# Performance work log

Measured on AMD Instinct MI355X. Metric: run time of the kernel, lower is better.

Reference implementation:

```python
import jax, jax.numpy as jnp
import numpy as np

TEMPERATURE = 0.07
BALANCE = 1.0


def _l2norm(x, eps=1e-12):
    return x / jnp.maximum(jnp.linalg.norm(x, axis=1, keepdims=True), eps)


def setup_inputs() -> dict:
    key = jax.random.key(0)
    k1, k2 = jax.random.split(key)
    B, K, D = 32768, 8192, 384
    features = _l2norm(jax.random.normal(k1, (B, D), dtype=jnp.float32))
    centroids = jax.random.normal(k2, (K, D), dtype=jnp.float32)
    return {"features": features, "centroids": centroids}


def reference(features, centroids):
    # centroids: [K, D] learnable; features: [B, D] sampled batch (L2-normalized)
    c = _l2norm(centroids)
    # chunked matmul + exp + row-max in source == single fused GEMM+exp+max here
    prod_exp = jnp.exp(jnp.matmul(features, c.T) / TEMPERATURE)  # [B, K]
    pos_k = jnp.argmax(prod_exp, axis=1)                          # [B] int
    prod_exp_pos = jnp.max(prod_exp, axis=1)                      # [B]
    # centroid-centroid similarity; first operand is detached in source
    cent_exp = jnp.exp(jnp.matmul(jax.lax.stop_gradient(c), c.T) / TEMPERATURE)  # [K, K]
    cent_sum = jnp.sum(cent_exp, axis=0)                          # [K]
    J = jnp.log(prod_exp_pos) - jnp.log(prod_exp_pos + cent_sum[pos_k] * BALANCE)
    return -jnp.mean(J)
```

## Files before the change

### kernel.cpp

```cpp
#include <hip/hip_runtime.h>
#include <math.h>

constexpr int B = 32768;
constexpr int K = 8192;
constexpr int D = 384;
constexpr float INV_T = 1.0f / 0.07f;

constexpr int TILE_B = 24 * 64 * 16;

typedef int    int8v    __attribute__((ext_vector_type(8)));
typedef float  floatx16 __attribute__((ext_vector_type(16)));

__global__ __launch_bounds__(64) void normalize_k(const float* __restrict__ cent,
                                                  unsigned char* __restrict__ cbs) {
    const int row = blockIdx.x, lane = threadIdx.x;
    const float* src = cent + (size_t)row * D;
    float4 x = {0.f, 0.f, 0.f, 0.f}, y = {0.f, 0.f, 0.f, 0.f};
    if (lane < 48) {
        x = *(const float4*)(src + lane * 8);
        y = *(const float4*)(src + lane * 8 + 4);
    }
    float ss = x.x * x.x + x.y * x.y + x.z * x.z + x.w * x.w
             + y.x * y.x + y.y * y.y + y.z * y.z + y.w * y.w;
#pragma unroll
    for (int off = 32; off > 0; off >>= 1) ss += __shfl_down(ss, off, 64);
    ss = __shfl(ss, 0, 64);
    const float inv = 1.0f / fmaxf(sqrtf(ss), 1e-12f);
    if (lane < 48) {
        int w0 = __builtin_amdgcn_cvt_pk_fp8_f32(x.x * inv, x.y * inv, 0, false);
        w0 = __builtin_amdgcn_cvt_pk_fp8_f32(x.z * inv, x.w * inv, w0, true);
        int w1 = __builtin_amdgcn_cvt_pk_fp8_f32(y.x * inv, y.y * inv, 0, false);
        w1 = __builtin_amdgcn_cvt_pk_fp8_f32(y.z * inv, y.w * inv, w1, true);
        char* dst = (char*)cbs + (size_t)(row >> 6) * TILE_B
                  + ((size_t)(lane >> 1) * 64 + (row & 63)) * 16 + (lane & 1) * 8;
        *(int2*)dst = make_int2(w0, w1);
    }
}

__device__ __forceinline__ int8v read_frag(const char* base, int t, int half) {
    const uint4 b0 = *(const uint4*)(base + (4 * t + 2 * half) * 1024);
    const uint4 b1 = *(const uint4*)(base + (4 * t + 2 * half + 1) * 1024);
    int8v f;
    f[0] = b0.x; f[1] = b0.y; f[2] = b0.z; f[3] = b0.w;
    f[4] = b1.x; f[5] = b1.y; f[6] = b1.z; f[7] = b1.w;
    return f;
}

__global__ __launch_bounds__(256, 2) void centsum_k(const unsigned char* __restrict__ cbs,
                                                    float* __restrict__ cent_sum) {
    const int tid = threadIdx.x, lane = tid & 63, wave = tid >> 6;
    const int wm = wave >> 1, wn = wave & 1;
    const int l31 = lane & 31, half = lane >> 5;
    const int rb = blockIdx.x >> 3, ch = blockIdx.x & 7;
    const int stag = (rb & 3) * 4;

    int8v afr[2][6];
#pragma unroll
    for (int s = 0; s < 2; ++s) {
        const char* abase = (const char*)cbs + (size_t)(rb * 2 + wm) * TILE_B
                          + (s * 32 + l31) * 16;
#pragma unroll
        for (int t = 0; t < 6; ++t) afr[s][t] = read_frag(abase, t, half);
    }

    float rs[2][16];
#pragma unroll
    for (int s = 0; s < 2; ++s)
#pragma unroll
        for (int r = 0; r < 16; ++r) rs[s][r] = 0.f;

#pragma unroll 2
    for (int it = 0; it < 16; ++it) {
        const int tile = ch * 16 + ((stag + it) & 15);
        const char* gb = (const char*)cbs + (size_t)tile * TILE_B
                       + (wn * 32 + l31) * 16;
        int8v bfr[6];
#pragma unroll
        for (int t = 0; t < 6; ++t) bfr[t] = read_frag(gb, t, half);
        floatx16 acc0, acc1;
#pragma unroll
        for (int r = 0; r < 16; ++r) { acc0[r] = 0.f; acc1[r] = 0.f; }
#pragma unroll
        for (int t = 0; t < 6; ++t) {
            acc0 = __builtin_amdgcn_mfma_scale_f32_32x32x64_f8f6f4(
                       afr[0][t], bfr[t], acc0, 0, 0, 0, 127, 0, 127);
            acc1 = __builtin_amdgcn_mfma_scale_f32_32x32x64_f8f6f4(
                       afr[1][t], bfr[t], acc1, 0, 0, 0, 127, 0, 127);
        }
#pragma unroll
        for (int r = 0; r < 16; ++r) {
            rs[0][r] += __expf(acc0[r] * INV_T);
            rs[1][r] += __expf(acc1[r] * INV_T);
        }
    }

#pragma unroll
    for (int s = 0; s < 2; ++s)
#pragma unroll
        for (int r = 0; r < 16; ++r) {
            float v = rs[s][r];
#pragma unroll
            for (int off = 1; off < 32; off <<= 1) v += __shfl_xor(v, off, 64);
            if (l31 == 0) {
                const int rowl = (r & 3) + 8 * (r >> 2) + 4 * half;
                atomicAdd(&cent_sum[rb * 128 + wm * 64 + s * 32 + rowl], v);
            }
        }
}

__global__ __launch_bounds__(256, 2) void rowmax_k(const float* __restrict__ f,
                                                   const unsigned char* __restrict__ cbs,
                                                   float* __restrict__ row_max2,
                                                   int* __restrict__ row_arg2) {
    __shared__ float rv[128 * 2];
    __shared__ int   ri[128 * 2];
    const int tid = threadIdx.x, lane = tid & 63, wave = tid >> 6;
    const int wm = wave >> 1, wn = wave & 1;
    const int l31 = lane & 31, half = lane >> 5;
    const int rb = blockIdx.x >> 1, ch = blockIdx.x & 1;
    const int stag = (rb & 7) * 8;

    int8v afr[2][6];
    const int rowbase = rb * 128 + wm * 64;
#pragma unroll
    for (int s = 0; s < 2; ++s) {
        const float* arow = f + (size_t)(rowbase + s * 32 + l31) * D;
#pragma unroll
        for (int t = 0; t < 6; ++t) {
            const float* p = arow + t * 64 + half * 32;
            int8v a;
#pragma unroll
            for (int q = 0; q < 8; ++q) {
                const float4 v = *(const float4*)(p + q * 4);
                int w = __builtin_amdgcn_cvt_pk_fp8_f32(v.x, v.y, 0, false);
                w = __builtin_amdgcn_cvt_pk_fp8_f32(v.z, v.w, w, true);
                a[q] = w;
            }
            afr[s][t] = a;
        }
    }

    float bv[2][16];
    int   bi[2][16];
#pragma unroll
    for (int s = 0; s < 2; ++s)
#pragma unroll
        for (int r = 0; r < 16; ++r) { bv[s][r] = -INFINITY; bi[s][r] = 0; }

#pragma unroll 2
    for (int it = 0; it < 64; ++it) {
        const int tile = ch * 64 + ((stag + it) & 63);
        const char* gb = (const char*)cbs + (size_t)tile * TILE_B
                       + (wn * 32 + l31) * 16;
        int8v bfr[6];
#pragma unroll
        for (int t = 0; t < 6; ++t) bfr[t] = read_frag(gb, t, half);
        floatx16 acc0, acc1;
#pragma unroll
        for (int r = 0; r < 16; ++r) { acc0[r] = 0.f; acc1[r] = 0.f; }
#pragma unroll
        for (int t = 0; t < 6; ++t) {
            acc0 = __builtin_amdgcn_mfma_scale_f32_32x32x64_f8f6f4(
                       afr[0][t], bfr[t], acc0, 0, 0, 0, 127, 0, 127);
            acc1 = __builtin_amdgcn_mfma_scale_f32_32x32x64_f8f6f4(
                       afr[1][t], bfr[t], acc1, 0, 0, 0, 127, 0, 127);
        }
        const int curCol = tile * 64 + wn * 32 + l31;
#pragma unroll
        for (int r = 0; r < 16; ++r) {
            if (acc0[r] > bv[0][r]) { bv[0][r] = acc0[r]; bi[0][r] = curCol; }
            if (acc1[r] > bv[1][r]) { bv[1][r] = acc1[r]; bi[1][r] = curCol; }
        }
    }

#pragma unroll
    for (int s = 0; s < 2; ++s)
#pragma unroll
        for (int r = 0; r < 16; ++r) {
            float v = bv[s][r]; int ix = bi[s][r];
#pragma unroll
            for (int off = 1; off < 32; off <<= 1) {
                const float ov = __shfl_xor(v, off, 64);
                const int   oi = __shfl_xor(ix, off, 64);
                if (ov > v || (ov == v && oi < ix)) { v = ov; ix = oi; }
            }
            bv[s][r] = v; bi[s][r] = ix;
        }

    if (l31 == 0) {
#pragma unroll
        for (int s = 0; s < 2; ++s)
#pragma unroll
            for (int r = 0; r < 16; ++r) {
                const int row = wm * 64 + s * 32 + (r & 3) + 8 * (r >> 2) + 4 * half;
                rv[row * 2 + wn] = bv[s][r];
                ri[row * 2 + wn] = bi[s][r];
            }
    }
    __syncthreads();
    if (tid < 128) {
        const float v0 = rv[tid * 2], v1 = rv[tid * 2 + 1];
        const int   i0 = ri[tid * 2], i1 = ri[tid * 2 + 1];
        const bool take1 = (v1 > v0) || (v1 == v0 && i1 < i0);
        row_max2[(size_t)(rb * 128 + tid) * 2 + ch] = take1 ? v1 : v0;
        row_arg2[(size_t)(rb * 128 + tid) * 2 + ch] = take1 ? i1 : i0;
    }
}

__global__ __launch_bounds__(256) void loss_k(const float* __restrict__ row_max2,
                                              const int* __restrict__ row_arg2,
                                              const float* __restrict__ cent_sum,
                                              float* __restrict__ out) {
    __shared__ float red[256];
    const int tid = threadIdx.x;
    float s = 0.f;
    for (int b = blockIdx.x * 256 + tid; b < B; b += gridDim.x * 256) {
        const float m0 = row_max2[(size_t)b * 2], m1 = row_max2[(size_t)b * 2 + 1];
        const bool take1 = m1 > m0;
        const float m = take1 ? m1 : m0;
        const int ix = row_arg2[(size_t)b * 2 + (take1 ? 1 : 0)];
        s += log1pf(cent_sum[ix] * expf(-m * INV_T));
    }
    red[tid] = s;
    __syncthreads();
    for (int off = 128; off > 0; off >>= 1) {
        if (tid < off) red[tid] += red[tid + off];
        __syncthreads();
    }
    if (tid == 0) atomicAdd(out, red[0] / (float)B);
}

extern "C" void kernel_launch(void* const* d_in, const int* in_sizes, int n_in,
                              void* d_out, int out_size, void* d_ws, size_t ws_size,
                              hipStream_t stream) {
    const float* features  = (const float*)d_in[0];
    const float* centroids = (const float*)d_in[1];
    float* out = (float*)d_out;

    char* ws = (char*)d_ws;
    unsigned char* cbs = (unsigned char*)ws;
    float* cent_sum = (float*)(ws + (size_t)(K / 64) * TILE_B);
    float* row_max2 = cent_sum + K;
    int*   row_arg2 = (int*)(row_max2 + 2 * B);

    hipMemsetAsync(cent_sum, 0, K * sizeof(float), stream);
    hipMemsetAsync(out, 0, sizeof(float), stream);
    normalize_k<<<K, 64, 0, stream>>>(centroids, cbs);
    centsum_k<<<(K / 128) * 8, 256, 0, stream>>>(cbs, cent_sum);
    rowmax_k<<<(B / 128) * 2, 256, 0, stream>>>(features, cbs, row_max2, row_arg2);
    loss_k<<<64, 256, 0, stream>>>(row_max2, row_arg2, cent_sum, out);
}
```

Measured before the change: 240.5 us.

## Double per-block row tile to 256 so each B fragment feeds four MFMAs

```diff
diff --git a/kernel.cpp b/kernel.cpp
--- a/kernel.cpp
+++ b/kernel.cpp
@@ -46,7 +46,7 @@
     return f;
 }
 
-__global__ __launch_bounds__(256, 2) void centsum_k(const unsigned char* __restrict__ cbs,
+__global__ __launch_bounds__(256, 1) void centsum_k(const unsigned char* __restrict__ cbs,
                                                     float* __restrict__ cent_sum) {
     const int tid = threadIdx.x, lane = tid & 63, wave = tid >> 6;
     const int wm = wave >> 1, wn = wave & 1;
@@ -54,22 +54,22 @@
     const int rb = blockIdx.x >> 3, ch = blockIdx.x & 7;
     const int stag = (rb & 3) * 4;
 
-    int8v afr[2][6];
-#pragma unroll
-    for (int s = 0; s < 2; ++s) {
-        const char* abase = (const char*)cbs + (size_t)(rb * 2 + wm) * TILE_B
-                          + (s * 32 + l31) * 16;
+    int8v afr[4][6];
+#pragma unroll
+    for (int s = 0; s < 4; ++s) {
+        const char* abase = (const char*)cbs
+                          + (size_t)(rb * 4 + wm * 2 + (s >> 1)) * TILE_B
+                          + ((s & 1) * 32 + l31) * 16;
 #pragma unroll
         for (int t = 0; t < 6; ++t) afr[s][t] = read_frag(abase, t, half);
     }
 
-    float rs[2][16];
-#pragma unroll
-    for (int s = 0; s < 2; ++s)
+    float rs[4][16];
+#pragma unroll
+    for (int s = 0; s < 4; ++s)
 #pragma unroll
         for (int r = 0; r < 16; ++r) rs[s][r] = 0.f;
 
-#pragma unroll 2
     for (int it = 0; it < 16; ++it) {
         const int tile = ch * 16 + ((stag + it) & 15);
         const char* gb = (const char*)cbs + (size_t)tile * TILE_B
@@ -77,25 +77,26 @@
         int8v bfr[6];
 #pragma unroll
         for (int t = 0; t < 6; ++t) bfr[t] = read_frag(gb, t, half);
-        floatx16 acc0, acc1;
-#pragma unroll
-        for (int r = 0; r < 16; ++r) { acc0[r] = 0.f; acc1[r] = 0.f; }
+        floatx16 acc[4];
+#pragma unroll
+        for (int s = 0; s < 4; ++s)
+#pragma unroll
+            for (int r = 0; r < 16; ++r) acc[s][r] = 0.f;
 #pragma unroll
         for (int t = 0; t < 6; ++t) {
-            acc0 = __builtin_amdgcn_mfma_scale_f32_32x32x64_f8f6f4(
-                       afr[0][t], bfr[t], acc0, 0, 0, 0, 127, 0, 127);
-            acc1 = __builtin_amdgcn_mfma_scale_f32_32x32x64_f8f6f4(
-                       afr[1][t], bfr[t], acc1, 0, 0, 0, 127, 0, 127);
-        }
-#pragma unroll
-        for (int r = 0; r < 16; ++r) {
-            rs[0][r] += __expf(acc0[r] * INV_T);
-            rs[1][r] += __expf(acc1[r] * INV_T);
-        }
-    }
-
-#pragma unroll
-    for (int s = 0; s < 2; ++s)
+#pragma unroll
+            for (int s = 0; s < 4; ++s)
+                acc[s] = __builtin_amdgcn_mfma_scale_f32_32x32x64_f8f6f4(
+                             afr[s][t], bfr[t], acc[s], 0, 0, 0, 127, 0, 127);
+        }
+#pragma unroll
+        for (int s = 0; s < 4; ++s)
+#pragma unroll
+            for (int r = 0; r < 16; ++r) rs[s][r] += __expf(acc[s][r] * INV_T);
+    }
+
+#pragma unroll
+    for (int s = 0; s < 4; ++s)
 #pragma unroll
         for (int r = 0; r < 16; ++r) {
             float v = rs[s][r];
@@ -103,27 +104,27 @@
             for (int off = 1; off < 32; off <<= 1) v += __shfl_xor(v, off, 64);
             if (l31 == 0) {
                 const int rowl = (r & 3) + 8 * (r >> 2) + 4 * half;
-                atomicAdd(&cent_sum[rb * 128 + wm * 64 + s * 32 + rowl], v);
-            }
-        }
-}
-
-__global__ __launch_bounds__(256, 2) void rowmax_k(const float* __restrict__ f,
+                atomicAdd(&cent_sum[rb * 256 + wm * 128 + s * 32 + rowl], v);
+            }
+        }
+}
+
+__global__ __launch_bounds__(256, 1) void rowmax_k(const float* __restrict__ f,
                                                    const unsigned char* __restrict__ cbs,
                                                    float* __restrict__ row_max2,
                                                    int* __restrict__ row_arg2) {
-    __shared__ float rv[128 * 2];
-    __shared__ int   ri[128 * 2];
+    __shared__ float rv[256 * 2];
+    __shared__ int   ri[256 * 2];
     const int tid = threadIdx.x, lane = tid & 63, wave = tid >> 6;
     const int wm = wave >> 1, wn = wave & 1;
     const int l31 = lane & 31, half = lane >> 5;
     const int rb = blockIdx.x >> 1, ch = blockIdx.x & 1;
     const int stag = (rb & 7) * 8;
 
-    int8v afr[2][6];
-    const int rowbase = rb * 128 + wm * 64;
-#pragma unroll
-    for (int s = 0; s < 2; ++s) {
+    int8v afr[4][6];
+    const int rowbase = rb * 256 + wm * 128;
+#pragma unroll
+    for (int s = 0; s < 4; ++s) {
         const float* arow = f + (size_t)(rowbase + s * 32 + l31) * D;
 #pragma unroll
         for (int t = 0; t < 6; ++t) {
@@ -140,14 +141,13 @@
         }
     }
 
-    float bv[2][16];
-    int   bi[2][16];
-#pragma unroll
-    for (int s = 0; s < 2; ++s)
+    float bv[4][16];
+    int   bi[4][16];
+#pragma unroll
+    for (int s = 0; s < 4; ++s)
 #pragma unroll
         for (int r = 0; r < 16; ++r) { bv[s][r] = -INFINITY; bi[s][r] = 0; }
 
-#pragma unroll 2
     for (int it = 0; it < 64; ++it) {
         const int tile = ch * 64 + ((stag + it) & 63);
         const char* gb = (const char*)cbs + (size_t)tile * TILE_B
@@ -155,26 +155,30 @@
         int8v bfr[6];
 #pragma unroll
         for (int t = 0; t < 6; ++t) bfr[t] = read_frag(gb, t, half);
-        floatx16 acc0, acc1;
-#pragma unroll
-        for (int r = 0; r < 16; ++r) { acc0[r] = 0.f; acc1[r] = 0.f; }
+        floatx16 acc[4];
+#pragma unroll
+        for (int s = 0; s < 4; ++s)
+#pragma unroll
+            for (int r = 0; r < 16; ++r) acc[s][r] = 0.f;
 #pragma unroll
         for (int t = 0; t < 6; ++t) {
-            acc0 = __builtin_amdgcn_mfma_scale_f32_32x32x64_f8f6f4(
-                       afr[0][t], bfr[t], acc0, 0, 0, 0, 127, 0, 127);
-            acc1 = __builtin_amdgcn_mfma_scale_f32_32x32x64_f8f6f4(
-                       afr[1][t], bfr[t], acc1, 0, 0, 0, 127, 0, 127);
+#pragma unroll
+            for (int s = 0; s < 4; ++s)
+                acc[s] = __builtin_amdgcn_mfma_scale_f32_32x32x64_f8f6f4(
+                             afr[s][t], bfr[t], acc[s], 0, 0, 0, 127, 0, 127);
         }
         const int curCol = tile * 64 + wn * 32 + l31;
 #pragma unroll
-        for (int r = 0; r < 16; ++r) {
-            if (acc0[r] > bv[0][r]) { bv[0][r] = acc0[r]; bi[0][r] = curCol; }
-            if (acc1[r] > bv[1][r]) { bv[1][r] = acc1[r]; bi[1][r] = curCol; }
-        }
-    }
-
-#pragma unroll
-    for (int s = 0; s < 2; ++s)
+        for (int s = 0; s < 4; ++s)
+#pragma unroll
+            for (int r = 0; r < 16; ++r) {
+                const float v = acc[s][r];
+                if (v > bv[s][r]) { bv[s][r] = v; bi[s][r] = curCol; }
+            }
+    }
+
+#pragma unroll
+    for (int s = 0; s < 4; ++s)
 #pragma unroll
         for (int r = 0; r < 16; ++r) {
             float v = bv[s][r]; int ix = bi[s][r];
@@ -189,21 +193,21 @@
 
     if (l31 == 0) {
 #pragma unroll
-        for (int s = 0; s < 2; ++s)
+        for (int s = 0; s < 4; ++s)
 #pragma unroll
             for (int r = 0; r < 16; ++r) {
-                const int row = wm * 64 + s * 32 + (r & 3) + 8 * (r >> 2) + 4 * half;
+                const int row = wm * 128 + s * 32 + (r & 3) + 8 * (r >> 2) + 4 * half;
                 rv[row * 2 + wn] = bv[s][r];
                 ri[row * 2 + wn] = bi[s][r];
             }
     }
     __syncthreads();
-    if (tid < 128) {
+    {
         const float v0 = rv[tid * 2], v1 = rv[tid * 2 + 1];
         const int   i0 = ri[tid * 2], i1 = ri[tid * 2 + 1];
         const bool take1 = (v1 > v0) || (v1 == v0 && i1 < i0);
-        row_max2[(size_t)(rb * 128 + tid) * 2 + ch] = take1 ? v1 : v0;
-        row_arg2[(size_t)(rb * 128 + tid) * 2 + ch] = take1 ? i1 : i0;
+        row_max2[(size_t)(rb * 256 + tid) * 2 + ch] = take1 ? v1 : v0;
+        row_arg2[(size_t)(rb * 256 + tid) * 2 + ch] = take1 ? i1 : i0;
     }
 }
 
@@ -246,7 +250,7 @@
     hipMemsetAsync(cent_sum, 0, K * sizeof(float), stream);
     hipMemsetAsync(out, 0, sizeof(float), stream);
     normalize_k<<<K, 64, 0, stream>>>(centroids, cbs);
-    centsum_k<<<(K / 128) * 8, 256, 0, stream>>>(cbs, cent_sum);
-    rowmax_k<<<(B / 128) * 2, 256, 0, stream>>>(features, cbs, row_max2, row_arg2);
+    centsum_k<<<(K / 256) * 8, 256, 0, stream>>>(cbs, cent_sum);
+    rowmax_k<<<(B / 256) * 2, 256, 0, stream>>>(features, cbs, row_max2, row_arg2);
     loss_k<<<64, 256, 0, stream>>>(row_max2, row_arg2, cent_sum, out);
 }
```

Result: slower. 319.4 us (+32.8%).

## Fuse centsum and rowmax into one launch, split columns four ways, add ballot-guarded argmax

Applied to the files above, without the earlier changes.

```diff
diff --git a/kernel.cpp b/kernel.cpp
--- a/kernel.cpp
+++ b/kernel.cpp
@@ -7,6 +7,9 @@
 constexpr float INV_T = 1.0f / 0.07f;
 
 constexpr int TILE_B = 24 * 64 * 16;
+
+constexpr int N_CS_BLK = 512;
+constexpr int N_RM_BLK = (B / 128) * 4;
 
 typedef int    int8v    __attribute__((ext_vector_type(8)));
 typedef float  floatx16 __attribute__((ext_vector_type(16)));
@@ -46,12 +49,12 @@
     return f;
 }
 
-__global__ __launch_bounds__(256, 2) void centsum_k(const unsigned char* __restrict__ cbs,
-                                                    float* __restrict__ cent_sum) {
+__device__ __forceinline__ void centsum_body(const unsigned char* __restrict__ cbs,
+                                             float* __restrict__ cent_sum, int bid) {
     const int tid = threadIdx.x, lane = tid & 63, wave = tid >> 6;
     const int wm = wave >> 1, wn = wave & 1;
     const int l31 = lane & 31, half = lane >> 5;
-    const int rb = blockIdx.x >> 3, ch = blockIdx.x & 7;
+    const int rb = bid >> 3, ch = bid & 7;
     const int stag = (rb & 3) * 4;
 
     int8v afr[2][6];
@@ -108,17 +111,16 @@
         }
 }
 
-__global__ __launch_bounds__(256, 2) void rowmax_k(const float* __restrict__ f,
-                                                   const unsigned char* __restrict__ cbs,
-                                                   float* __restrict__ row_max2,
-                                                   int* __restrict__ row_arg2) {
-    __shared__ float rv[128 * 2];
-    __shared__ int   ri[128 * 2];
+__device__ __forceinline__ void rowmax_body(const float* __restrict__ f,
+                                            const unsigned char* __restrict__ cbs,
+                                            float* __restrict__ row_max4,
+                                            int* __restrict__ row_arg4,
+                                            int bid, float* rv, int* ri) {
     const int tid = threadIdx.x, lane = tid & 63, wave = tid >> 6;
     const int wm = wave >> 1, wn = wave & 1;
     const int l31 = lane & 31, half = lane >> 5;
-    const int rb = blockIdx.x >> 1, ch = blockIdx.x & 1;
-    const int stag = (rb & 7) * 8;
+    const int rb = bid >> 2, ch = bid & 3;
+    const int stag = (rb & 7) * 4;
 
     int8v afr[2][6];
     const int rowbase = rb * 128 + wm * 64;
@@ -148,8 +150,8 @@
         for (int r = 0; r < 16; ++r) { bv[s][r] = -INFINITY; bi[s][r] = 0; }
 
 #pragma unroll 2
-    for (int it = 0; it < 64; ++it) {
-        const int tile = ch * 64 + ((stag + it) & 63);
+    for (int it = 0; it < 32; ++it) {
+        const int tile = ch * 32 + ((stag + it) & 31);
         const char* gb = (const char*)cbs + (size_t)tile * TILE_B
                        + (wn * 32 + l31) * 16;
         int8v bfr[6];
@@ -168,8 +170,14 @@
         const int curCol = tile * 64 + wn * 32 + l31;
 #pragma unroll
         for (int r = 0; r < 16; ++r) {
-            if (acc0[r] > bv[0][r]) { bv[0][r] = acc0[r]; bi[0][r] = curCol; }
-            if (acc1[r] > bv[1][r]) { bv[1][r] = acc1[r]; bi[1][r] = curCol; }
+            const float v0 = acc0[r];
+            if (__ballot(v0 > bv[0][r])) {
+                if (v0 > bv[0][r]) { bv[0][r] = v0; bi[0][r] = curCol; }
+            }
+            const float v1 = acc1[r];
+            if (__ballot(v1 > bv[1][r])) {
+                if (v1 > bv[1][r]) { bv[1][r] = v1; bi[1][r] = curCol; }
+            }
         }
     }
 
@@ -202,23 +210,39 @@
         const float v0 = rv[tid * 2], v1 = rv[tid * 2 + 1];
         const int   i0 = ri[tid * 2], i1 = ri[tid * 2 + 1];
         const bool take1 = (v1 > v0) || (v1 == v0 && i1 < i0);
-        row_max2[(size_t)(rb * 128 + tid) * 2 + ch] = take1 ? v1 : v0;
-        row_arg2[(size_t)(rb * 128 + tid) * 2 + ch] = take1 ? i1 : i0;
-    }
-}
-
-__global__ __launch_bounds__(256) void loss_k(const float* __restrict__ row_max2,
-                                              const int* __restrict__ row_arg2,
+        row_max4[(size_t)(rb * 128 + tid) * 4 + ch] = take1 ? v1 : v0;
+        row_arg4[(size_t)(rb * 128 + tid) * 4 + ch] = take1 ? i1 : i0;
+    }
+}
+
+__global__ __launch_bounds__(256, 3) void fused_k(const float* __restrict__ f,
+                                                  const unsigned char* __restrict__ cbs,
+                                                  float* __restrict__ cent_sum,
+                                                  float* __restrict__ row_max4,
+                                                  int* __restrict__ row_arg4) {
+    __shared__ float rv[256];
+    __shared__ int   ri[256];
+    if (blockIdx.x < N_CS_BLK)
+        centsum_body(cbs, cent_sum, blockIdx.x);
+    else
+        rowmax_body(f, cbs, row_max4, row_arg4, blockIdx.x - N_CS_BLK, rv, ri);
+}
+
+__global__ __launch_bounds__(256) void loss_k(const float* __restrict__ row_max4,
+                                              const int* __restrict__ row_arg4,
                                               const float* __restrict__ cent_sum,
                                               float* __restrict__ out) {
     __shared__ float red[256];
     const int tid = threadIdx.x;
     float s = 0.f;
     for (int b = blockIdx.x * 256 + tid; b < B; b += gridDim.x * 256) {
-        const float m0 = row_max2[(size_t)b * 2], m1 = row_max2[(size_t)b * 2 + 1];
-        const bool take1 = m1 > m0;
-        const float m = take1 ? m1 : m0;
-        const int ix = row_arg2[(size_t)b * 2 + (take1 ? 1 : 0)];
+        float m = row_max4[(size_t)b * 4];
+        int   ix = row_arg4[(size_t)b * 4];
+#pragma unroll
+        for (int c = 1; c < 4; ++c) {
+            const float mc = row_max4[(size_t)b * 4 + c];
+            if (mc > m) { m = mc; ix = row_arg4[(size_t)b * 4 + c]; }
+        }
         s += log1pf(cent_sum[ix] * expf(-m * INV_T));
     }
     red[tid] = s;
@@ -240,13 +264,13 @@
     char* ws = (char*)d_ws;
     unsigned char* cbs = (unsigned char*)ws;
     float* cent_sum = (float*)(ws + (size_t)(K / 64) * TILE_B);
-    float* row_max2 = cent_sum + K;
-    int*   row_arg2 = (int*)(row_max2 + 2 * B);
+    float* row_max4 = cent_sum + K;
+    int*   row_arg4 = (int*)(row_max4 + 4 * (size_t)B);
 
     hipMemsetAsync(cent_sum, 0, K * sizeof(float), stream);
     hipMemsetAsync(out, 0, sizeof(float), stream);
     normalize_k<<<K, 64, 0, stream>>>(centroids, cbs);
-    centsum_k<<<(K / 128) * 8, 256, 0, stream>>>(cbs, cent_sum);
-    rowmax_k<<<(B / 128) * 2, 256, 0, stream>>>(features, cbs, row_max2, row_arg2);
-    loss_k<<<64, 256, 0, stream>>>(row_max2, row_arg2, cent_sum, out);
-}
+    fused_k<<<N_CS_BLK + N_RM_BLK, 256, 0, stream>>>(features, cbs, cent_sum,
+                                                     row_max4, row_arg4);
+    loss_k<<<64, 256, 0, stream>>>(row_max4, row_arg4, cent_sum, out);
+}
```

New measurement: 673.5 us. 180% more time.
